# Optimization experiments

Hardware: AMD Instinct MI355X
Metric: run time of the kernel (lower is better)

## Reference

```python
import jax, jax.numpy as jnp
import numpy as np

DIM = 192


def _conv1x1(x, w, b):
    # x: [B, C_in, H, W], w: [C_out, C_in], b: [C_out]
    return jnp.einsum('bchw,oc->bohw', x, w) + b[None, :, None, None]


def setup_inputs() -> dict:
    key = jax.random.key(0)
    ks = jax.random.split(key, 7)
    B, T, C, H, W = 4, 16, DIM, 56, 56
    scale = 1.0 / np.sqrt(2 * C)
    return {
        'video': jax.random.normal(ks[0], (B, T, C, H, W), dtype=jnp.float32),
        'w_z': jax.random.normal(ks[1], (C, 2 * C), dtype=jnp.float32) * scale,
        'b_z': jax.random.normal(ks[2], (C,), dtype=jnp.float32) * scale,
        'w_r': jax.random.normal(ks[3], (C, 2 * C), dtype=jnp.float32) * scale,
        'b_r': jax.random.normal(ks[4], (C,), dtype=jnp.float32) * scale,
        'w_h': jax.random.normal(ks[5], (C, 2 * C), dtype=jnp.float32) * scale,
        'b_h': jax.random.normal(ks[6], (C,), dtype=jnp.float32) * scale,
    }


def reference(video, w_z, b_z, w_r, b_r, w_h, b_h):
    # video: [B, T, C, H, W]
    h0 = jnp.zeros_like(video[:, 0])  # [B, C, H, W]

    def step(h, x):
        xh = jnp.concatenate([x, h], axis=1)  # [B, 2C, H, W]
        z = jax.nn.sigmoid(_conv1x1(xh, w_z, b_z))
        r = jax.nn.sigmoid(_conv1x1(xh, w_r, b_r))
        xrh = jnp.concatenate([x, r * h], axis=1)
        h_new = (1.0 - z) * h + z * jnp.tanh(_conv1x1(xrh, w_h, b_h))
        return h_new, h_new

    # scan over time axis
    _, out = jax.lax.scan(step, h0, jnp.moveaxis(video, 1, 0))
    return jnp.moveaxis(out, 0, 1)  # [B, T, C, H, W]
```

## Files before the change

kernel.cpp:

```cpp
#include <hip/hip_runtime.h>
#include <cstdint>
#include <cstddef>

typedef _Float16 f16;
typedef _Float16 half8 __attribute__((ext_vector_type(8)));
typedef _Float16 half4 __attribute__((ext_vector_type(4)));
typedef float f32x4 __attribute__((ext_vector_type(4)));
typedef unsigned int u32;
typedef u32 u32x4 __attribute__((ext_vector_type(4)));

constexpr int CDIM = 192, HW = 3136, NBAT = 4, TSTEPS = 16;
constexpr int MTOT = NBAT * HW;
constexpr int NSUB = MTOT / 16;
constexpr int NCHUNK = MTOT / 32;

constexpr size_t OFF_WX = 0;
constexpr size_t SZ_WX  = (size_t)6*36*64*8*2;
constexpr size_t OFF_WHB = OFF_WX + SZ_WX;
constexpr size_t SZ_WHB  = (size_t)12*3*6*64*8*2;
constexpr size_t OFF_U  = OFF_WHB + SZ_WHB;
constexpr size_t SZ_U   = (size_t)16*NSUB*12*3*64*4*2;
constexpr size_t NEED   = OFF_U + SZ_U;

constexpr size_t FB_WZR = 0;
constexpr size_t FB_SZ_WZR = (size_t)384*384*2;
constexpr size_t FB_WH  = FB_WZR + FB_SZ_WZR;


__global__ void pack_w(const float* __restrict__ wz, const float* __restrict__ wr,
                       const float* __restrict__ wh, char* __restrict__ ws) {
    int idx = blockIdx.x * 256 + threadIdx.x;
    if (idx >= 221184) return;
    f16* dst;
    int lane, i, k, c, gate;
    if (idx < 110592) {
        i = idx & 7; lane = (idx >> 3) & 63;
        int ktnt = idx >> 9, kt = ktnt / 36, nt = ktnt % 36;
        int n576 = nt * 16 + (lane & 15);
        gate = n576 / 192; c = n576 % 192;
        k = kt * 32 + (lane >> 4) * 8 + i;
        dst = (f16*)(ws + OFF_WX) + idx;
    } else {
        int j = idx - 110592;
        i = j & 7; lane = (j >> 3) & 63;
        int a = j >> 9, kt = a % 6, b = a / 6;
        gate = b % 3; int nsl = b / 3;
        c = nsl * 16 + (lane & 15);
        k = 192 + kt * 32 + (lane >> 4) * 8 + i;
        dst = (f16*)(ws + OFF_WHB) + j;
    }
    const float* W = (gate == 0) ? wz : (gate == 1) ? wr : wh;
    *dst = (f16)W[c * 384 + k];
}

__global__ __launch_bounds__(512, 2) void xproj(
    const float* __restrict__ video, char* __restrict__ ws,
    const float* __restrict__ bz, const float* __restrict__ br,
    const float* __restrict__ bh) {
    __shared__ __align__(16) char AX[2][24576];
    const f16* WX = (const f16*)(ws + OFF_WX);
    f16* U = (f16*)(ws + OFF_U);
    const int tid = threadIdx.x, w = tid >> 6, lane = tid & 63;
    const int l15 = lane & 15, lg = lane >> 4;
    const int mt = blockIdx.x;
    const int bb = mt / 49, hw0 = (mt % 49) * 64;
    const int t0 = blockIdx.y * 2;
    const int mg = w >> 2, nw = w & 3;
    const int swsh = (lane & 7) << 4;
    const int slot = (l15 & 7) << 4;

#pragma unroll
    for (int p = 0; p < 2; ++p) {
        const float* vs = video + ((size_t)(bb * TSTEPS + t0 + p) * CDIM) * HW + hw0 + lane;
#pragma unroll
        for (int g = 0; g < 3; ++g) {
            half8 hv;
#pragma unroll
            for (int j = 0; j < 8; ++j)
                hv[j] = (f16)__builtin_nontemporal_load(vs + (size_t)(w * 24 + g * 8 + j) * HW);
            *(half8*)(AX[p] + lane * 384 + ((w * 48 + g * 16) ^ swsh)) = hv;
        }
    }
    float vb[9];
#pragma unroll
    for (int r = 0; r < 9; ++r) {
        int n576 = nw * 144 + r * 16 + l15;
        int gate = n576 / 192, c = n576 % 192;
        vb[r] = (gate == 0 ? bz : (gate == 1 ? br : bh))[c];
    }
    __syncthreads();

    f32x4 acc[4][9];
#pragma unroll
    for (int i = 0; i < 4; ++i)
#pragma unroll
        for (int r = 0; r < 9; ++r)
#pragma unroll
            for (int q = 0; q < 4; ++q) acc[i][r][q] = vb[r];

#pragma unroll
    for (int kt = 0; kt < 6; ++kt) {
        half8 a[4];
#pragma unroll
        for (int i = 0; i < 4; ++i)
            a[i] = *(const half8*)(AX[mg] + (i * 16 + l15) * 384 + ((kt * 64 + lg * 16) ^ slot));
#pragma unroll
        for (int r = 0; r < 9; ++r) {
            half8 bf = *(const half8*)(WX + ((size_t)(kt * 36 + nw * 9 + r) * 64 + lane) * 8);
#pragma unroll
            for (int i = 0; i < 4; ++i)
                acc[i][r] = __builtin_amdgcn_mfma_f32_16x16x32_f16(a[i], bf, acc[i][r], 0, 0, 0);
        }
    }
    const int t = t0 + mg;
#pragma unroll
    for (int r = 0; r < 9; ++r) {
        int nb = nw * 9 + r;
        int gate = nb / 12, nsl = nb % 12;
#pragma unroll
        for (int i = 0; i < 4; ++i) {
            half4 hq;
#pragma unroll
            for (int q = 0; q < 4; ++q) hq[q] = (f16)acc[i][r][q];
            int sub = mt * 4 + i;
            f16* up = U + (((size_t)t * NSUB + sub) * 36 + (size_t)nsl * 3 + gate) * 256
                        + (size_t)lane * 4;
            __builtin_nontemporal_store(hq, (half4*)up);
        }
    }
}

__global__ __launch_bounds__(768, 3) void recur(const char* __restrict__ ws,
                                                float* __restrict__ dout) {
    __shared__ __align__(16) char AH[12288], RH[12288];
    const f16* WHB = (const f16*)(ws + OFF_WHB);
    const f16* U = (const f16*)(ws + OFF_U);
    const int tid = threadIdx.x, wv = tid >> 6, lane = tid & 63;
    const int l15 = lane & 15, lg = lane >> 4;
    const int ch = blockIdx.x;
    const int bb = ch / 98, hw0 = (ch % 98) * 32;
    const int slot = (l15 & 7) << 4;

    half8 wz_[6], wr_[6], wh_[6];
    {
        const f16* base = WHB + (size_t)wv * 9216 + lane * 8;
#pragma unroll
        for (int kt = 0; kt < 6; ++kt) {
            wz_[kt] = *(const half8*)(base + (0 * 6 + kt) * 512);
            wr_[kt] = *(const half8*)(base + (1 * 6 + kt) * 512);
            wh_[kt] = *(const half8*)(base + (2 * 6 + kt) * 512);
        }
    }
    {
        u32x4 z = {0, 0, 0, 0};
        *(u32x4*)(AH + tid * 16) = z;
    }
    __syncthreads();

    const f16* ub = U + ((size_t)ch * 2 * 36 + (size_t)wv * 3) * 256 + (size_t)lane * 4;
    constexpr size_t UT = (size_t)NSUB * 36 * 256;
    half4 uz0 = __builtin_nontemporal_load((const half4*)(ub));
    half4 ur0 = __builtin_nontemporal_load((const half4*)(ub + 256));
    half4 uh0 = __builtin_nontemporal_load((const half4*)(ub + 512));
    half4 uz1 = __builtin_nontemporal_load((const half4*)(ub + 36 * 256));
    half4 ur1 = __builtin_nontemporal_load((const half4*)(ub + 36 * 256 + 256));
    half4 uh1 = __builtin_nontemporal_load((const half4*)(ub + 36 * 256 + 512));

    const int ohw = tid & 31, ocg = tid >> 5;
    const int obyte = ohw * 384 + ((ocg * 16) ^ ((ohw & 7) << 4));
    float* obase = dout + (size_t)bb * TSTEPS * CDIM * HW + (size_t)ocg * 8 * HW + hw0 + ohw;

#pragma unroll 1
    for (int t = 0; t < TSTEPS; ++t) {
        f32x4 az[2], ar[2];
#pragma unroll
        for (int i = 0; i < 2; ++i)
#pragma unroll
            for (int q = 0; q < 4; ++q) { az[i][q] = 0.f; ar[i][q] = 0.f; }
#pragma unroll
        for (int kt = 0; kt < 6; ++kt) {
            half8 a0 = *(const half8*)(AH + l15 * 384 + ((kt * 64 + lg * 16) ^ slot));
            half8 a1 = *(const half8*)(AH + (16 + l15) * 384 + ((kt * 64 + lg * 16) ^ slot));
            az[0] = __builtin_amdgcn_mfma_f32_16x16x32_f16(a0, wz_[kt], az[0], 0, 0, 0);
            az[1] = __builtin_amdgcn_mfma_f32_16x16x32_f16(a1, wz_[kt], az[1], 0, 0, 0);
            ar[0] = __builtin_amdgcn_mfma_f32_16x16x32_f16(a0, wr_[kt], ar[0], 0, 0, 0);
            ar[1] = __builtin_amdgcn_mfma_f32_16x16x32_f16(a1, wr_[kt], ar[1], 0, 0, 0);
        }
        float zg[2][4], ho[2][4];
#pragma unroll
        for (int i = 0; i < 2; ++i)
#pragma unroll
            for (int q = 0; q < 4; ++q) {
                int row = i * 16 + lg * 4 + q;
                int cb = 2 * (wv * 16 + l15), sw = (row & 7) << 4;
                float uzv = (float)(i ? uz1[q] : uz0[q]);
                float urv = (float)(i ? ur1[q] : ur0[q]);
                float z = 1.f / (1.f + __expf(-(az[i][q] + uzv)));
                float r = 1.f / (1.f + __expf(-(ar[i][q] + urv)));
                float h = (float)*(const f16*)(AH + row * 384 + (cb ^ sw));
                zg[i][q] = z; ho[i][q] = (1.f - z) * h;
                *(f16*)(RH + row * 384 + (cb ^ sw)) = (f16)(r * h);
            }
        __syncthreads();

        half4 nz0 = uz0, nr0 = ur0, nh0 = uh0, nz1 = uz1, nr1 = ur1, nh1 = uh1;
        if (t + 1 < TSTEPS) {
            const f16* un = ub + (size_t)(t + 1) * UT;
            nz0 = __builtin_nontemporal_load((const half4*)(un));
            nr0 = __builtin_nontemporal_load((const half4*)(un + 256));
            nh0 = __builtin_nontemporal_load((const half4*)(un + 512));
            nz1 = __builtin_nontemporal_load((const half4*)(un + 36 * 256));
            nr1 = __builtin_nontemporal_load((const half4*)(un + 36 * 256 + 256));
            nh1 = __builtin_nontemporal_load((const half4*)(un + 36 * 256 + 512));
        }

        f32x4 ah[2];
#pragma unroll
        for (int i = 0; i < 2; ++i)
#pragma unroll
            for (int q = 0; q < 4; ++q) ah[i][q] = 0.f;
#pragma unroll
        for (int kt = 0; kt < 6; ++kt) {
            half8 a0 = *(const half8*)(RH + l15 * 384 + ((kt * 64 + lg * 16) ^ slot));
            half8 a1 = *(const half8*)(RH + (16 + l15) * 384 + ((kt * 64 + lg * 16) ^ slot));
            ah[0] = __builtin_amdgcn_mfma_f32_16x16x32_f16(a0, wh_[kt], ah[0], 0, 0, 0);
            ah[1] = __builtin_amdgcn_mfma_f32_16x16x32_f16(a1, wh_[kt], ah[1], 0, 0, 0);
        }
#pragma unroll
        for (int i = 0; i < 2; ++i)
#pragma unroll
            for (int q = 0; q < 4; ++q) {
                int row = i * 16 + lg * 4 + q;
                int cb = 2 * (wv * 16 + l15), sw = (row & 7) << 4;
                float uhv = (float)(i ? uh1[q] : uh0[q]);
                float e = __expf(2.f * (ah[i][q] + uhv));
                float th = 1.f - 2.f / (e + 1.f);
                *(f16*)(AH + row * 384 + (cb ^ sw)) = (f16)(ho[i][q] + zg[i][q] * th);
            }
        __syncthreads();

        {
            half8 hv = *(const half8*)(AH + obyte);
            float* ob = obase + (size_t)t * CDIM * HW;
#pragma unroll
            for (int j = 0; j < 8; ++j)
                __builtin_nontemporal_store((float)hv[j], ob + (size_t)j * HW);
        }
        uz0 = nz0; ur0 = nr0; uh0 = nh0; uz1 = nz1; ur1 = nr1; uh1 = nh1;
    }
}


__global__ void pack5(const float* __restrict__ wz, const float* __restrict__ wr,
                      const float* __restrict__ wh, char* __restrict__ ws) {
    int idx = blockIdx.x * 256 + threadIdx.x;
    const int ZRT = 384 * 384;
    int n, k, NT;
    float w;
    f16* dst;
    if (idx < ZRT) {
        n = idx / 384; k = idx - n * 384;
        w = (n < 192) ? wz[n * 384 + k] : wr[(n - 192) * 384 + k];
        dst = (f16*)(ws + FB_WZR); NT = 24;
    } else {
        int j = idx - ZRT;
        if (j >= 192 * 384) return;
        n = j / 384; k = j - n * 384;
        w = wh[n * 384 + k];
        dst = (f16*)(ws + FB_WH); NT = 12;
    }
    int kt = k >> 5, g = (k >> 3) & 3, i = k & 7, nt = n >> 4;
    int lane = (g << 4) | (n & 15);
    dst[((size_t)(kt * NT + nt) * 64 + lane) * 8 + i] = (f16)w;
}

__global__ __launch_bounds__(256, 2) void gru_fb(
    const float* __restrict__ video,
    const f16* __restrict__ wZR, const f16* __restrict__ wH,
    const float* __restrict__ bz, const float* __restrict__ br,
    const float* __restrict__ bh, float* __restrict__ dout) {
    __shared__ __align__(16) char smem[73728];
    char* AX = smem;
    char* AH = smem + 24576;
    char* RH = smem + 49152;
    const int tid = threadIdx.x, w = tid >> 6, lane = tid & 63;
    const int l15 = lane & 15, lg = lane >> 4;
    const int mt = blockIdx.x, bb = mt / 49, hw0 = (mt % 49) * 64;
    const int slot = (l15 & 7) << 4;
    const int swsh = (lane & 7) << 4;
    const float* vbase = video + (size_t)bb * TSTEPS * CDIM * HW + hw0 + lane;
    float* obase = dout + (size_t)bb * TSTEPS * CDIM * HW + hw0 + lane;
    float vbz[3], vbr[3], vbh[3];
#pragma unroll
    for (int r = 0; r < 3; ++r) {
        int c = w * 48 + r * 16 + l15;
        vbz[r] = bz[c]; vbr[r] = br[c]; vbh[r] = bh[c];
    }
    {
        half8 zz = {};
#pragma unroll
        for (int i = 0; i < 6; ++i) *(half8*)(AH + tid * 96 + i * 16) = zz;
#pragma unroll
        for (int g = 0; g < 6; ++g) {
            half8 hv;
#pragma unroll
            for (int j = 0; j < 8; ++j)
                hv[j] = (f16)__builtin_nontemporal_load(vbase + (size_t)(w * 48 + g * 8 + j) * HW);
            *(half8*)(AX + lane * 384 + ((w * 96 + g * 16) ^ swsh)) = hv;
        }
    }
    __syncthreads();
#pragma unroll 1
    for (int t = 0; t < TSTEPS; ++t) {
        f32x4 az[4][3], ar[4][3];
#pragma unroll
        for (int i = 0; i < 4; ++i)
#pragma unroll
            for (int r = 0; r < 3; ++r)
#pragma unroll
                for (int q = 0; q < 4; ++q) { az[i][r][q] = 0.f; ar[i][r][q] = 0.f; }
#pragma unroll
        for (int kt = 0; kt < 12; ++kt) {
            const char* ab = (kt < 6) ? AX : AH;
            int kb = (kt % 6) * 64 + lg * 16;
            half8 a[4];
#pragma unroll
            for (int i = 0; i < 4; ++i)
                a[i] = *(const half8*)(ab + (i * 16 + l15) * 384 + (kb ^ slot));
#pragma unroll
            for (int r = 0; r < 3; ++r) {
                half8 bzf = *(const half8*)(wZR + ((size_t)(kt * 24 + w * 3 + r) * 64 + lane) * 8);
                half8 brf = *(const half8*)(wZR + ((size_t)(kt * 24 + 12 + w * 3 + r) * 64 + lane) * 8);
#pragma unroll
                for (int i = 0; i < 4; ++i)
                    az[i][r] = __builtin_amdgcn_mfma_f32_16x16x32_f16(a[i], bzf, az[i][r], 0, 0, 0);
#pragma unroll
                for (int i = 0; i < 4; ++i)
                    ar[i][r] = __builtin_amdgcn_mfma_f32_16x16x32_f16(a[i], brf, ar[i][r], 0, 0, 0);
            }
        }
        float xn[6][8];
        if (t + 1 < TSTEPS) {
            const float* vs = vbase + (size_t)(t + 1) * CDIM * HW;
#pragma unroll
            for (int g = 0; g < 6; ++g)
#pragma unroll
                for (int j = 0; j < 8; ++j)
                    xn[g][j] = __builtin_nontemporal_load(vs + (size_t)(w * 48 + g * 8 + j) * HW);
        }
#pragma unroll
        for (int i = 0; i < 4; ++i)
#pragma unroll
            for (int r = 0; r < 3; ++r)
#pragma unroll
                for (int q = 0; q < 4; ++q) {
                    int row = i * 16 + lg * 4 + q;
                    int cb = 2 * (w * 48 + r * 16 + l15), sw = (row & 7) << 4;
                    float rg = 1.f / (1.f + __expf(-(ar[i][r][q] + vbr[r])));
                    float hv = (float)*(const f16*)(AH + row * 384 + (cb ^ sw));
                    *(f16*)(RH + row * 384 + (cb ^ sw)) = (f16)(rg * hv);
                }
        __syncthreads();
        f32x4 ac[4][3];
#pragma unroll
        for (int i = 0; i < 4; ++i)
#pragma unroll
            for (int r = 0; r < 3; ++r)
#pragma unroll
                for (int q = 0; q < 4; ++q) ac[i][r][q] = 0.f;
#pragma unroll
        for (int kt = 0; kt < 12; ++kt) {
            const char* ab = (kt < 6) ? AX : RH;
            int kb = (kt % 6) * 64 + lg * 16;
            half8 a[4];
#pragma unroll
            for (int i = 0; i < 4; ++i)
                a[i] = *(const half8*)(ab + (i * 16 + l15) * 384 + (kb ^ slot));
#pragma unroll
            for (int r = 0; r < 3; ++r) {
                half8 bf = *(const half8*)(wH + ((size_t)(kt * 12 + w * 3 + r) * 64 + lane) * 8);
#pragma unroll
                for (int i = 0; i < 4; ++i)
                    ac[i][r] = __builtin_amdgcn_mfma_f32_16x16x32_f16(a[i], bf, ac[i][r], 0, 0, 0);
            }
        }
#pragma unroll
        for (int i = 0; i < 4; ++i)
#pragma unroll
            for (int r = 0; r < 3; ++r)
#pragma unroll
                for (int q = 0; q < 4; ++q) {
                    int row = i * 16 + lg * 4 + q;
                    int cb = 2 * (w * 48 + r * 16 + l15), sw = (row & 7) << 4;
                    float zgv = 1.f / (1.f + __expf(-(az[i][r][q] + vbz[r])));
                    float e = __expf(2.f * (ac[i][r][q] + vbh[r]));
                    float th = 1.f - 2.f / (e + 1.f);
                    float hold = (float)*(const f16*)(AH + row * 384 + (cb ^ sw));
                    *(f16*)(AH + row * 384 + (cb ^ sw)) = (f16)((1.f - zgv) * hold + zgv * th);
                }
        __syncthreads();
        {
            float* ob = obase + (size_t)t * CDIM * HW;
#pragma unroll
            for (int g = 0; g < 6; ++g) {
                half8 hv = *(const half8*)(AH + lane * 384 + ((w * 96 + g * 16) ^ swsh));
#pragma unroll
                for (int j = 0; j < 8; ++j)
                    __builtin_nontemporal_store((float)hv[j], ob + (size_t)(w * 48 + g * 8 + j) * HW);
            }
            if (t + 1 < TSTEPS) {
#pragma unroll
                for (int g = 0; g < 6; ++g) {
                    half8 o;
#pragma unroll
                    for (int j = 0; j < 8; ++j) o[j] = (f16)xn[g][j];
                    *(half8*)(AX + lane * 384 + ((w * 96 + g * 16) ^ swsh)) = o;
                }
            }
        }
        __syncthreads();
    }
}

extern "C" void kernel_launch(void* const* d_in, const int* in_sizes, int n_in,
                              void* d_out, int out_size, void* d_ws, size_t ws_size,
                              hipStream_t stream) {
    const float* video = (const float*)d_in[0];
    const float* wz = (const float*)d_in[1];
    const float* bz = (const float*)d_in[2];
    const float* wr = (const float*)d_in[3];
    const float* br = (const float*)d_in[4];
    const float* wh = (const float*)d_in[5];
    const float* bh = (const float*)d_in[6];
    char* ws = (char*)d_ws;
    float* dout = (float*)d_out;

    if (ws_size >= NEED) {
        pack_w<<<864, 256, 0, stream>>>(wz, wr, wh, ws);
        xproj<<<dim3(196, 8), 512, 0, stream>>>(video, ws, bz, br, bh);
        recur<<<NCHUNK, 768, 0, stream>>>(ws, dout);
    } else {
        pack5<<<864, 256, 0, stream>>>(wz, wr, wh, ws);
        gru_fb<<<196, 256, 0, stream>>>(video, (const f16*)(ws + FB_WZR),
                                        (const f16*)(ws + FB_WH), bz, br, bh, dout);
    }
}
```

Baseline: 238.0 us.

## Split recurrence into 16-pixel blocks and keep hidden state in registers

The recurrent kernel now handles 16 spatial positions per block instead of 32. This doubles the grid to 784 blocks and halves the MFMA work and LDS per block, giving more parallelism for the serial time loop. Each lane keeps its own hidden-state values in fp32 registers, so it no longer rereads them from LDS, and it writes output as one float4 per step instead of going through an LDS transpose. Nontemporal hints are also dropped on the U stores and loads. The trade-off is that each block reloads the weight fragments into registers, roughly doubling total weight traffic, and does less MFMA work between barriers.

After: 252.7 us. 6.2% more time.

```diff
diff --git a/kernel.cpp b/kernel.cpp
--- a/kernel.cpp
+++ b/kernel.cpp
@@ -12,7 +12,6 @@
 constexpr int CDIM = 192, HW = 3136, NBAT = 4, TSTEPS = 16;
 constexpr int MTOT = NBAT * HW;
 constexpr int NSUB = MTOT / 16;
-constexpr int NCHUNK = MTOT / 32;
 
 constexpr size_t OFF_WX = 0;
 constexpr size_t SZ_WX  = (size_t)6*36*64*8*2;
@@ -125,21 +124,22 @@
             int sub = mt * 4 + i;
             f16* up = U + (((size_t)t * NSUB + sub) * 36 + (size_t)nsl * 3 + gate) * 256
                         + (size_t)lane * 4;
-            __builtin_nontemporal_store(hq, (half4*)up);
+            *(half4*)up = hq;
         }
     }
 }
 
 __global__ __launch_bounds__(768, 3) void recur(const char* __restrict__ ws,
                                                 float* __restrict__ dout) {
-    __shared__ __align__(16) char AH[12288], RH[12288];
+    __shared__ __align__(16) char AH[6144], RH[6144];
     const f16* WHB = (const f16*)(ws + OFF_WHB);
     const f16* U = (const f16*)(ws + OFF_U);
     const int tid = threadIdx.x, wv = tid >> 6, lane = tid & 63;
     const int l15 = lane & 15, lg = lane >> 4;
-    const int ch = blockIdx.x;
-    const int bb = ch / 98, hw0 = (ch % 98) * 32;
+    const int sub = blockIdx.x;
+    const int bb = sub / 196, hw0 = (sub % 196) * 16;
     const int slot = (l15 & 7) << 4;
+    const int col = wv * 16 + l15;
 
     half8 wz_[6], wr_[6], wh_[6];
     {
@@ -151,102 +151,68 @@
             wh_[kt] = *(const half8*)(base + (2 * 6 + kt) * 512);
         }
     }
-    {
-        u32x4 z = {0, 0, 0, 0};
-        *(u32x4*)(AH + tid * 16) = z;
-    }
+    *(uint64_t*)(AH + tid * 8) = 0ull;
     __syncthreads();
 
-    const f16* ub = U + ((size_t)ch * 2 * 36 + (size_t)wv * 3) * 256 + (size_t)lane * 4;
+    const f16* ub = U + ((size_t)sub * 36 + (size_t)wv * 3) * 256 + (size_t)lane * 4;
     constexpr size_t UT = (size_t)NSUB * 36 * 256;
-    half4 uz0 = __builtin_nontemporal_load((const half4*)(ub));
-    half4 ur0 = __builtin_nontemporal_load((const half4*)(ub + 256));
-    half4 uh0 = __builtin_nontemporal_load((const half4*)(ub + 512));
-    half4 uz1 = __builtin_nontemporal_load((const half4*)(ub + 36 * 256));
-    half4 ur1 = __builtin_nontemporal_load((const half4*)(ub + 36 * 256 + 256));
-    half4 uh1 = __builtin_nontemporal_load((const half4*)(ub + 36 * 256 + 512));
-
-    const int ohw = tid & 31, ocg = tid >> 5;
-    const int obyte = ohw * 384 + ((ocg * 16) ^ ((ohw & 7) << 4));
-    float* obase = dout + (size_t)bb * TSTEPS * CDIM * HW + (size_t)ocg * 8 * HW + hw0 + ohw;
+    half4 uz = *(const half4*)(ub);
+    half4 ur = *(const half4*)(ub + 256);
+    half4 uh = *(const half4*)(ub + 512);
+
+    float h_own[4] = {0.f, 0.f, 0.f, 0.f};
+    const int cb = (2 * col);
+    float* ob = dout + ((size_t)(bb * TSTEPS) * CDIM + col) * HW + hw0 + lg * 4;
 
 #pragma unroll 1
     for (int t = 0; t < TSTEPS; ++t) {
-        f32x4 az[2], ar[2];
-#pragma unroll
-        for (int i = 0; i < 2; ++i)
-#pragma unroll
-            for (int q = 0; q < 4; ++q) { az[i][q] = 0.f; ar[i][q] = 0.f; }
+        f32x4 az = {0.f, 0.f, 0.f, 0.f}, ar = {0.f, 0.f, 0.f, 0.f};
 #pragma unroll
         for (int kt = 0; kt < 6; ++kt) {
             half8 a0 = *(const half8*)(AH + l15 * 384 + ((kt * 64 + lg * 16) ^ slot));
-            half8 a1 = *(const half8*)(AH + (16 + l15) * 384 + ((kt * 64 + lg * 16) ^ slot));
-            az[0] = __builtin_amdgcn_mfma_f32_16x16x32_f16(a0, wz_[kt], az[0], 0, 0, 0);
-            az[1] = __builtin_amdgcn_mfma_f32_16x16x32_f16(a1, wz_[kt], az[1], 0, 0, 0);
-            ar[0] = __builtin_amdgcn_mfma_f32_16x16x32_f16(a0, wr_[kt], ar[0], 0, 0, 0);
-            ar[1] = __builtin_amdgcn_mfma_f32_16x16x32_f16(a1, wr_[kt], ar[1], 0, 0, 0);
-        }
-        float zg[2][4], ho[2][4];
-#pragma unroll
-        for (int i = 0; i < 2; ++i)
-#pragma unroll
-            for (int q = 0; q < 4; ++q) {
-                int row = i * 16 + lg * 4 + q;
-                int cb = 2 * (wv * 16 + l15), sw = (row & 7) << 4;
-                float uzv = (float)(i ? uz1[q] : uz0[q]);
-                float urv = (float)(i ? ur1[q] : ur0[q]);
-                float z = 1.f / (1.f + __expf(-(az[i][q] + uzv)));
-                float r = 1.f / (1.f + __expf(-(ar[i][q] + urv)));
-                float h = (float)*(const f16*)(AH + row * 384 + (cb ^ sw));
-                zg[i][q] = z; ho[i][q] = (1.f - z) * h;
-                *(f16*)(RH + row * 384 + (cb ^ sw)) = (f16)(r * h);
-            }
+            az = __builtin_amdgcn_mfma_f32_16x16x32_f16(a0, wz_[kt], az, 0, 0, 0);
+            ar = __builtin_amdgcn_mfma_f32_16x16x32_f16(a0, wr_[kt], ar, 0, 0, 0);
+        }
+        float zg[4], ho[4];
+#pragma unroll
+        for (int q = 0; q < 4; ++q) {
+            int row = lg * 4 + q;
+            int b = cb ^ ((row & 7) << 4);
+            float z = 1.f / (1.f + __expf(-(az[q] + (float)uz[q])));
+            float r = 1.f / (1.f + __expf(-(ar[q] + (float)ur[q])));
+            zg[q] = z; ho[q] = (1.f - z) * h_own[q];
+            *(f16*)(RH + row * 384 + b) = (f16)(r * h_own[q]);
+        }
         __syncthreads();
 
-        half4 nz0 = uz0, nr0 = ur0, nh0 = uh0, nz1 = uz1, nr1 = ur1, nh1 = uh1;
+        half4 nz = uz, nr = ur, nh = uh;
         if (t + 1 < TSTEPS) {
             const f16* un = ub + (size_t)(t + 1) * UT;
-            nz0 = __builtin_nontemporal_load((const half4*)(un));
-            nr0 = __builtin_nontemporal_load((const half4*)(un + 256));
-            nh0 = __builtin_nontemporal_load((const half4*)(un + 512));
-            nz1 = __builtin_nontemporal_load((const half4*)(un + 36 * 256));
-            nr1 = __builtin_nontemporal_load((const half4*)(un + 36 * 256 + 256));
-            nh1 = __builtin_nontemporal_load((const half4*)(un + 36 * 256 + 512));
-        }
-
-        f32x4 ah[2];
-#pragma unroll
-        for (int i = 0; i < 2; ++i)
-#pragma unroll
-            for (int q = 0; q < 4; ++q) ah[i][q] = 0.f;
+            nz = *(const half4*)(un);
+            nr = *(const half4*)(un + 256);
+            nh = *(const half4*)(un + 512);
+        }
+
+        f32x4 ah = {0.f, 0.f, 0.f, 0.f};
 #pragma unroll
         for (int kt = 0; kt < 6; ++kt) {
             half8 a0 = *(const half8*)(RH + l15 * 384 + ((kt * 64 + lg * 16) ^ slot));
-            half8 a1 = *(const half8*)(RH + (16 + l15) * 384 + ((kt * 64 + lg * 16) ^ slot));
-            ah[0] = __builtin_amdgcn_mfma_f32_16x16x32_f16(a0, wh_[kt], ah[0], 0, 0, 0);
-            ah[1] = __builtin_amdgcn_mfma_f32_16x16x32_f16(a1, wh_[kt], ah[1], 0, 0, 0);
-        }
-#pragma unroll
-        for (int i = 0; i < 2; ++i)
-#pragma unroll
-            for (int q = 0; q < 4; ++q) {
-                int row = i * 16 + lg * 4 + q;
-                int cb = 2 * (wv * 16 + l15), sw = (row & 7) << 4;
-                float uhv = (float)(i ? uh1[q] : uh0[q]);
-                float e = __expf(2.f * (ah[i][q] + uhv));
-                float th = 1.f - 2.f / (e + 1.f);
-                *(f16*)(AH + row * 384 + (cb ^ sw)) = (f16)(ho[i][q] + zg[i][q] * th);
-            }
+            ah = __builtin_amdgcn_mfma_f32_16x16x32_f16(a0, wh_[kt], ah, 0, 0, 0);
+        }
+        f32x4 hv;
+#pragma unroll
+        for (int q = 0; q < 4; ++q) {
+            int row = lg * 4 + q;
+            int b = cb ^ ((row & 7) << 4);
+            float e = __expf(2.f * (ah[q] + (float)uh[q]));
+            float th = 1.f - 2.f / (e + 1.f);
+            float hn = ho[q] + zg[q] * th;
+            h_own[q] = hn; hv[q] = hn;
+            *(f16*)(AH + row * 384 + b) = (f16)hn;
+        }
+        __builtin_nontemporal_store(hv, (f32x4*)(ob + (size_t)t * CDIM * HW));
         __syncthreads();
-
-        {
-            half8 hv = *(const half8*)(AH + obyte);
-            float* ob = obase + (size_t)t * CDIM * HW;
-#pragma unroll
-            for (int j = 0; j < 8; ++j)
-                __builtin_nontemporal_store((float)hv[j], ob + (size_t)j * HW);
-        }
-        uz0 = nz0; ur0 = nr0; uh0 = nh0; uz1 = nz1; ur1 = nr1; uh1 = nh1;
+        uz = nz; ur = nr; uh = nh;
     }
 }
 
@@ -355,10 +321,10 @@
 #pragma unroll
                 for (int q = 0; q < 4; ++q) {
                     int row = i * 16 + lg * 4 + q;
-                    int cb = 2 * (w * 48 + r * 16 + l15), sw = (row & 7) << 4;
+                    int cb2 = 2 * (w * 48 + r * 16 + l15), sw = (row & 7) << 4;
                     float rg = 1.f / (1.f + __expf(-(ar[i][r][q] + vbr[r])));
-                    float hv = (float)*(const f16*)(AH + row * 384 + (cb ^ sw));
-                    *(f16*)(RH + row * 384 + (cb ^ sw)) = (f16)(rg * hv);
+                    float hvv = (float)*(const f16*)(AH + row * 384 + (cb2 ^ sw));
+                    *(f16*)(RH + row * 384 + (cb2 ^ sw)) = (f16)(rg * hvv);
                 }
         __syncthreads();
         f32x4 ac[4][3];
@@ -391,12 +357,12 @@
 #pragma unroll
                 for (int q = 0; q < 4; ++q) {
                     int row = i * 16 + lg * 4 + q;
-                    int cb = 2 * (w * 48 + r * 16 + l15), sw = (row & 7) << 4;
+                    int cb2 = 2 * (w * 48 + r * 16 + l15), sw = (row & 7) << 4;
                     float zgv = 1.f / (1.f + __expf(-(az[i][r][q] + vbz[r])));
                     float e = __expf(2.f * (ac[i][r][q] + vbh[r]));
                     float th = 1.f - 2.f / (e + 1.f);
-                    float hold = (float)*(const f16*)(AH + row * 384 + (cb ^ sw));
-                    *(f16*)(AH + row * 384 + (cb ^ sw)) = (f16)((1.f - zgv) * hold + zgv * th);
+                    float hold = (float)*(const f16*)(AH + row * 384 + (cb2 ^ sw));
+                    *(f16*)(AH + row * 384 + (cb2 ^ sw)) = (f16)((1.f - zgv) * hold + zgv * th);
                 }
         __syncthreads();
         {
@@ -438,7 +404,7 @@
     if (ws_size >= NEED) {
         pack_w<<<864, 256, 0, stream>>>(wz, wr, wh, ws);
         xproj<<<dim3(196, 8), 512, 0, stream>>>(video, ws, bz, br, bh);
-        recur<<<NCHUNK, 768, 0, stream>>>(ws, dout);
+        recur<<<NSUB, 768, 0, stream>>>(ws, dout);
     } else {
         pack5<<<864, 256, 0, stream>>>(wz, wr, wh, ws);
         gru_fb<<<196, 256, 0, stream>>>(video, (const f16*)(ws + FB_WZR),
```
